# Kernel optimization log

Hardware: AMD Instinct MI355X
Metric: run time of the kernel (lower is better)

Reference implementation:

```python
import jax, jax.numpy as jnp
import numpy as np

ALPHA = 0.25
GAMMA = 2.0
W_CLASS = W_BBOX = W_GIOU = W_MASK = W_DICE = W_PROJ = 1.0
EPS = 1e-8


def box_cxcywh_to_xyxy(b):
    cx, cy, w, h = jnp.split(b, 4, axis=-1)
    return jnp.concatenate([cx - 0.5 * w, cy - 0.5 * h, cx + 0.5 * w, cy + 0.5 * h], axis=-1)


def dice_coef(inputs, targets):
    # inputs: logits [N, D]; targets: binary [M, D]
    s = jax.nn.sigmoid(inputs)
    num = 2.0 * jnp.einsum('nd,md->nm', s, targets)
    den = s.sum(-1)[:, None] + targets.sum(-1)[None, :]
    return (num + 1.0) / (den + 1.0)  # [N, M]


def sigmoid_focal_coef(inputs, targets):
    # inputs: logits [N, D]; targets: binary [M, D] -> [N, M]
    x = inputs[:, None, :]
    t = targets[None, :, :]
    p = jax.nn.sigmoid(x)
    # BCE-with-logits, numerically stable
    ce = jnp.maximum(x, 0.0) - x * t + jnp.log1p(jnp.exp(-jnp.abs(x)))
    p_t = p * t + (1.0 - p) * (1.0 - t)
    alpha_t = ALPHA * t + (1.0 - ALPHA) * (1.0 - t)
    return (alpha_t * ce * (1.0 - p_t) ** GAMMA).mean(-1)


def giou_cost(src_xyxy, tgt_xyxy):
    # src [nf, nq, 4], tgt [nf, 1, 4] -> cost [nf, nq, 1]
    a1 = (src_xyxy[..., 2] - src_xyxy[..., 0]) * (src_xyxy[..., 3] - src_xyxy[..., 1])
    a2 = (tgt_xyxy[..., 2] - tgt_xyxy[..., 0]) * (tgt_xyxy[..., 3] - tgt_xyxy[..., 1])
    lt = jnp.maximum(src_xyxy[:, :, None, :2], tgt_xyxy[:, None, :, :2])
    rb = jnp.minimum(src_xyxy[:, :, None, 2:], tgt_xyxy[:, None, :, 2:])
    wh = jnp.clip(rb - lt, 0.0)
    inter = wh[..., 0] * wh[..., 1]
    union = a1[:, :, None] + a2[:, None, :] - inter
    iou = inter / union
    ltc = jnp.minimum(src_xyxy[:, :, None, :2], tgt_xyxy[:, None, :, :2])
    rbc = jnp.maximum(src_xyxy[:, :, None, 2:], tgt_xyxy[:, None, :, 2:])
    whc = jnp.clip(rbc - ltc, 0.0)
    areac = whc[..., 0] * whc[..., 1]
    giou = iou - (areac - union) / areac
    return -giou


def cost_matrix_one(logits, boxes, masks, tmask, tbox, tvalid):
    # logits [nf,nq,1], boxes [nf,nq,4], masks [nf,nq,H,W], tmask [nf,H,W], tbox [nf,4], tvalid [nf]
    p = jax.nn.sigmoid(logits[..., 0])  # [nf, nq]
    neg = (1.0 - ALPHA) * p ** GAMMA * (-jnp.log(1.0 - p + EPS))
    pos = ALPHA * (1.0 - p) ** GAMMA * (-jnp.log(p + EPS))
    w = (tvalid != 0).astype(p.dtype)  # valid-frame mask replaces python `continue`
    cost_class = (((pos - neg) * w[:, None]).sum(0) / w.sum())[:, None]  # [nq, 1]

    cost_bbox = jnp.abs(boxes[:, :, None, :] - tbox[:, None, None, :]).sum(-1).mean(0)  # [nq, 1]
    cost_giou = giou_cost(box_cxcywh_to_xyxy(boxes), box_cxcywh_to_xyxy(tbox[:, None, :])).mean(0)

    out_mask = jnp.transpose(masks, (1, 0, 2, 3))  # [nq, nf, H, W]
    nq = out_mask.shape[0]
    flat_src = out_mask.reshape(nq, -1)
    flat_tgt = tmask.reshape(1, -1)
    cost_mask = sigmoid_focal_coef(flat_src, flat_tgt)  # [nq, 1]
    cost_dice = -dice_coef(flat_src, flat_tgt)

    src_y = jnp.max(out_mask, axis=2, keepdims=True).reshape(nq, -1)  # [nq, nf*W]
    src_x = jnp.max(out_mask, axis=3, keepdims=True).reshape(nq, -1)  # [nq, nf*H]
    tgt_y = jnp.max(tmask[None], axis=2, keepdims=True).reshape(1, -1)
    tgt_x = jnp.max(tmask[None], axis=3, keepdims=True).reshape(1, -1)
    cost_proj = -0.5 * (dice_coef(src_y, tgt_y) + dice_coef(src_x, tgt_x))

    C = (W_CLASS * cost_class + W_BBOX * cost_bbox + W_GIOU * cost_giou
         + W_MASK * cost_mask + W_DICE * cost_dice + W_PROJ * cost_proj)
    return C  # [nq, 1]


def setup_inputs() -> dict:
    key = jax.random.key(0)
    k = jax.random.split(key, 6)
    bs, nf, nq, H, W = 2, 8, 300, 96, 96
    pred_logits = jax.random.normal(k[0], (bs, nf, nq, 1), dtype=jnp.float32)
    pred_boxes = jax.random.uniform(k[1], (bs, nf, nq, 4), dtype=jnp.float32)
    pred_masks = jax.random.normal(k[2], (bs, nf, nq, H, W), dtype=jnp.float32)
    target_masks = (jax.random.uniform(k[3], (bs, nf, H, W)) < 0.3).astype(jnp.float32)
    tgt_boxes = jax.random.uniform(k[4], (bs, nf, 4), dtype=jnp.float32)
    tgt_valid = jnp.ones((bs, nf), dtype=jnp.int32)
    valid_pad = jnp.zeros((bs, H, W), dtype=bool)
    return {"pred_logits": pred_logits, "pred_boxes": pred_boxes, "pred_masks": pred_masks,
            "target_masks": target_masks, "tgt_boxes": tgt_boxes, "tgt_valid": tgt_valid,
            "valid_pad": valid_pad}


def reference(pred_logits, pred_boxes, pred_masks, target_masks, tgt_boxes, tgt_valid, valid_pad):
    # zero out predictions over padded regions (masked_fill with valid[:, None, None])
    masks = jnp.where(valid_pad[:, None, None, :, :], 0.0, pred_masks)
    C = jax.vmap(cost_matrix_one)(pred_logits, pred_boxes, masks, target_masks, tgt_boxes, tgt_valid)
    src_ind = jnp.argmin(C, axis=1).astype(jnp.int64)  # [bs, 1]
    tgt_ind = jnp.zeros_like(src_ind)
    return C, src_ind, tgt_ind
```

## Files before the change

### kernel.cpp

```cpp
#include <hip/hip_runtime.h>
#include <math.h>

#define NF 8
#define NQ 300
#define HSZ 96
#define WSZ 96
#define HW (HSZ*WSZ)
#define DTOT (NF*HW)
#define NT 256
#define NBF 16

#define WS_TGTY 0
#define WS_TGTX 1536
#define WS_TSUM 3072
#define WS_YSUM 3088
#define WS_XSUM 3104
#define WS_PART 4096

__device__ __forceinline__ float sigmoid_fast(float x) {
    float e = __expf(-fabsf(x));
    float inv = __builtin_amdgcn_rcpf(1.f + e);
    return x >= 0.f ? inv : e * inv;
}

__device__ __forceinline__ float blockSum(float v, float* red) {
    #pragma unroll
    for (int off = 32; off > 0; off >>= 1) v += __shfl_down(v, off, 64);
    int wid = threadIdx.x >> 6, lane = threadIdx.x & 63;
    __syncthreads();
    if (lane == 0) red[wid] = v;
    __syncthreads();
    return red[0] + red[1] + red[2] + red[3];
}

__global__ __launch_bounds__(NT)
void targets_kernel(const float* __restrict__ tm, float* __restrict__ ws) {
    int bf = blockIdx.x, t = threadIdx.x;
    __shared__ float tile[HSZ * 97];
    __shared__ float red[4];
    const float* base = tm + (size_t)bf * HW;
    float tsum = 0.f;
    #pragma unroll
    for (int it = 0; it < 36; ++it) {
        int e = it * NT + t;
        float v = base[e];
        tsum += v;
        tile[e + e / 96] = v;
    }
    __syncthreads();
    float ysum = 0.f, xsum = 0.f;
    if (t < 96) {
        float m = -INFINITY;
        #pragma unroll 8
        for (int h = 0; h < HSZ; ++h) m = fmaxf(m, tile[h * 97 + t]);
        ws[WS_TGTY + bf * 96 + t] = m;
        ysum = m;
    } else if (t < 192) {
        int hh = t - 96;
        float m = -INFINITY;
        #pragma unroll 8
        for (int w = 0; w < WSZ; ++w) m = fmaxf(m, tile[hh * 97 + w]);
        ws[WS_TGTX + bf * 96 + hh] = m;
        xsum = m;
    }
    tsum = blockSum(tsum, red);
    ysum = blockSum(ysum, red);
    xsum = blockSum(xsum, red);
    if (t == 0) {
        ws[WS_TSUM + bf] = tsum;
        ws[WS_YSUM + bf] = ysum;
        ws[WS_XSUM + bf] = xsum;
    }
}

__global__ __launch_bounds__(NT, 8)
void partial_kernel(const float* __restrict__ masks, const float* __restrict__ tmask,
                    const unsigned char* __restrict__ vpad, const float* __restrict__ ws,
                    float* __restrict__ part) {
    int bf = blockIdx.x / NQ;
    int q  = blockIdx.x - bf * NQ;
    int b  = bf >> 3;
    int t  = threadIdx.x;

    __shared__ unsigned short tile[HSZ * 98];
    __shared__ float red[4];

    const float4* mrow = (const float4*)(masks + (size_t)(bf * NQ + q) * HW);
    const float4* trow = (const float4*)(tmask + (size_t)bf * HW);
    const unsigned* prow = (const unsigned*)(vpad + (size_t)b * HW);

    float focal = 0.f, dnum = 0.f, dden = 0.f;

    #pragma unroll
    for (int it = 0; it < 9; ++it) {
        int i4 = it * NT + t;
        float4 xv = mrow[i4];
        float4 tv = trow[i4];
        unsigned pv = prow[i4];
        int h = i4 / 24;
        int c = (i4 - h * 24) * 4;

        float xs[4] = {xv.x, xv.y, xv.z, xv.w};
        float ts[4] = {tv.x, tv.y, tv.z, tv.w};
        unsigned short us[4];
        #pragma unroll
        for (int j = 0; j < 4; ++j) {
            float x = ((pv >> (8 * j)) & 0xFFu) ? 0.f : xs[j];
            float tg = ts[j];
            float ee = __expf(-fabsf(x));
            float se = 1.f + ee;
            float inv = __builtin_amdgcn_rcpf(se);
            float s = x >= 0.f ? inv : ee * inv;
            float L = __logf(se);
            float ce = fmaxf(x, 0.f) - x * tg + L;
            float omp = s + tg - 2.f * s * tg;
            float at = 0.75f - 0.5f * tg;
            focal = fmaf(at * ce, omp * omp, focal);
            dnum = fmaf(s, tg, dnum);
            dden += s;
            us[j] = (unsigned short)(__float_as_uint(x) >> 16);
        }
        int ta = h * 98 + c;
        *(unsigned*)&tile[ta]     = (unsigned)us[0] | ((unsigned)us[1] << 16);
        *(unsigned*)&tile[ta + 2] = (unsigned)us[2] | ((unsigned)us[3] << 16);
    }
    __syncthreads();

    float pYn = 0.f, pYd = 0.f, pXn = 0.f, pXd = 0.f;
    if (t < 96) {
        float m = -INFINITY;
        #pragma unroll 8
        for (int h = 0; h < HSZ; ++h)
            m = fmaxf(m, __uint_as_float((unsigned)tile[h * 98 + t] << 16));
        float sg = sigmoid_fast(m);
        pYd = sg;
        pYn = sg * ws[WS_TGTY + bf * 96 + t];
    } else if (t < 192) {
        int hh = t - 96;
        float m = -INFINITY;
        #pragma unroll 8
        for (int w = 0; w < WSZ; ++w)
            m = fmaxf(m, __uint_as_float((unsigned)tile[hh * 98 + w] << 16));
        float sg = sigmoid_fast(m);
        pXd = sg;
        pXn = sg * ws[WS_TGTX + bf * 96 + hh];
    }

    focal = blockSum(focal, red);
    dnum  = blockSum(dnum, red);
    dden  = blockSum(dden, red);
    pYn   = blockSum(pYn, red);
    pYd   = blockSum(pYd, red);
    pXn   = blockSum(pXn, red);
    pXd   = blockSum(pXd, red);

    if (t == 0) {
        float* p = part + (size_t)blockIdx.x * 8;
        p[0] = focal; p[1] = dnum; p[2] = dden;
        p[3] = pYn;   p[4] = pYd;  p[5] = pXn;  p[6] = pXd;
    }
}

__global__ __launch_bounds__(NT)
void combine_kernel(const float* __restrict__ logits, const float* __restrict__ boxes,
                    const float* __restrict__ tbox, const int* __restrict__ tvalid,
                    const float* __restrict__ ws, float* __restrict__ out) {
    int gid = blockIdx.x * NT + threadIdx.x;
    if (gid >= 2 * NQ) return;
    int b = gid / NQ, q = gid - b * NQ;

    float focal = 0.f, dnum = 0.f, dden = 0.f;
    float pYn = 0.f, pYd = 0.f, pXn = 0.f, pXd = 0.f;
    float tsum = 0.f, ysum = 0.f, xsum = 0.f;
    #pragma unroll
    for (int f = 0; f < NF; ++f) {
        int bf = b * NF + f;
        const float* p = ws + WS_PART + (size_t)(bf * NQ + q) * 8;
        focal += p[0]; dnum += p[1]; dden += p[2];
        pYn += p[3]; pYd += p[4]; pXn += p[5]; pXd += p[6];
        tsum += ws[WS_TSUM + bf];
        ysum += ws[WS_YSUM + bf];
        xsum += ws[WS_XSUM + bf];
    }
    float cost_mask = focal / (float)DTOT;
    float cost_dice = -(2.f * dnum + 1.f) / (dden + tsum + 1.f);
    float coefY = (2.f * pYn + 1.f) / (pYd + ysum + 1.f);
    float coefX = (2.f * pXn + 1.f) / (pXd + xsum + 1.f);
    float cost_proj = -0.5f * (coefY + coefX);

    float wsum = 0.f, cls = 0.f, cb = 0.f, cg = 0.f;
    #pragma unroll
    for (int f = 0; f < NF; ++f) {
        float wv = (tvalid[b * NF + f] != 0) ? 1.f : 0.f;
        wsum += wv;
        float lg = logits[(b * NF + f) * NQ + q];
        float p = sigmoid_fast(lg);
        float negc = 0.75f * p * p * (-__logf(1.f - p + 1e-8f));
        float posc = 0.25f * (1.f - p) * (1.f - p) * (-__logf(p + 1e-8f));
        cls += (posc - negc) * wv;

        const float* bx = boxes + (size_t)((b * NF + f) * NQ + q) * 4;
        const float* tb = tbox + (b * NF + f) * 4;
        float cx = bx[0], cy = bx[1], bw = bx[2], bh = bx[3];
        float tcx = tb[0], tcy = tb[1], tbw = tb[2], tbh = tb[3];
        cb += fabsf(cx - tcx) + fabsf(cy - tcy) + fabsf(bw - tbw) + fabsf(bh - tbh);
        float sx1 = cx - 0.5f * bw, sy1 = cy - 0.5f * bh;
        float sx2 = cx + 0.5f * bw, sy2 = cy + 0.5f * bh;
        float tx1 = tcx - 0.5f * tbw, ty1 = tcy - 0.5f * tbh;
        float tx2 = tcx + 0.5f * tbw, ty2 = tcy + 0.5f * tbh;
        float a1 = (sx2 - sx1) * (sy2 - sy1), a2 = (tx2 - tx1) * (ty2 - ty1);
        float iw = fmaxf(fminf(sx2, tx2) - fmaxf(sx1, tx1), 0.f);
        float ih = fmaxf(fminf(sy2, ty2) - fmaxf(sy1, ty1), 0.f);
        float inter = iw * ih;
        float uni = a1 + a2 - inter;
        float iou = inter / uni;
        float cw = fmaxf(fmaxf(sx2, tx2) - fminf(sx1, tx1), 0.f);
        float chh = fmaxf(fmaxf(sy2, ty2) - fminf(sy1, ty1), 0.f);
        float areac = cw * chh;
        cg += -(iou - (areac - uni) / areac);
    }
    cls /= wsum;
    cb *= 0.125f;
    cg *= 0.125f;
    out[b * NQ + q] = cls + cb + cg + cost_mask + cost_dice + cost_proj;
}

__global__ __launch_bounds__(NT)
void argmin_kernel(float* __restrict__ out, int write_idx) {
    int b = blockIdx.x, t = threadIdx.x;
    float best = INFINITY;
    int bi = 0x7fffffff;
    for (int q = t; q < NQ; q += NT) {
        float v = out[b * NQ + q];
        if (v < best) { best = v; bi = q; }
    }
    #pragma unroll
    for (int off = 32; off > 0; off >>= 1) {
        float ov = __shfl_down(best, off, 64);
        int oi = __shfl_down(bi, off, 64);
        if (ov < best || (ov == best && oi < bi)) { best = ov; bi = oi; }
    }
    __shared__ float rv[4];
    __shared__ int ri[4];
    int wid = t >> 6, lane = t & 63;
    if (lane == 0) { rv[wid] = best; ri[wid] = bi; }
    __syncthreads();
    if (t == 0 && write_idx) {
        #pragma unroll
        for (int w = 1; w < 4; ++w) {
            if (rv[w] < best || (rv[w] == best && ri[w] < bi)) { best = rv[w]; bi = ri[w]; }
        }
        out[2 * NQ + b] = (float)bi;
        out[2 * NQ + 2 + b] = 0.f;
    }
}

extern "C" void kernel_launch(void* const* d_in, const int* in_sizes, int n_in,
                              void* d_out, int out_size, void* d_ws, size_t ws_size,
                              hipStream_t stream) {
    const float* logits = (const float*)d_in[0];
    const float* boxes  = (const float*)d_in[1];
    const float* masks  = (const float*)d_in[2];
    const float* tmask  = (const float*)d_in[3];
    const float* tbox   = (const float*)d_in[4];
    const int*   tvalid = (const int*)d_in[5];
    const unsigned char* vpad = (const unsigned char*)d_in[6];
    float* out = (float*)d_out;
    float* ws  = (float*)d_ws;

    targets_kernel<<<NBF, NT, 0, stream>>>(tmask, ws);
    partial_kernel<<<NBF * NQ, NT, 0, stream>>>(masks, tmask, vpad, ws, ws + WS_PART);
    combine_kernel<<<(2 * NQ + NT - 1) / NT, NT, 0, stream>>>(logits, boxes, tbox,
                                                              tvalid, ws, out);
    int write_idx = (out_size >= 2 * NQ + 4) ? 1 : 0;
    argmin_kernel<<<2, NT, 0, stream>>>(out, write_idx);
}
```

Baseline: 311.8 us.

## Bit-pack target and pad masks, batch reductions, merge combine with argmin

The targets kernel now also packs the binary target masks and padding masks into bitmasks using wave ballots. The partial kernel then reads these bits instead of full float targets and byte pad values, which is meant to cut its per-block global traffic to mostly the prediction masks. All nine float4 mask loads are issued up front, and the seven block reductions are batched into one shared-memory sync round. The combine and argmin kernels are fused into one two-block kernel, removing a launch but serialising the combine work over only 2 blocks.

```diff
diff --git a/kernel.cpp b/kernel.cpp
--- a/kernel.cpp
+++ b/kernel.cpp
@@ -5,8 +5,8 @@
 #define NQ 300
 #define HSZ 96
 #define WSZ 96
-#define HW (HSZ*WSZ)
-#define DTOT (NF*HW)
+#define HW 9216
+#define DTOT 73728
 #define NT 256
 #define NBF 16
 
@@ -15,7 +15,9 @@
 #define WS_TSUM 3072
 #define WS_YSUM 3088
 #define WS_XSUM 3104
-#define WS_PART 4096
+#define WS_TBITS 3200
+#define WS_PBITS 7808
+#define WS_PART  8448
 
 __device__ __forceinline__ float sigmoid_fast(float x) {
     float e = __expf(-fabsf(x));
@@ -23,21 +25,14 @@
     return x >= 0.f ? inv : e * inv;
 }
 
-__device__ __forceinline__ float blockSum(float v, float* red) {
-    #pragma unroll
-    for (int off = 32; off > 0; off >>= 1) v += __shfl_down(v, off, 64);
-    int wid = threadIdx.x >> 6, lane = threadIdx.x & 63;
-    __syncthreads();
-    if (lane == 0) red[wid] = v;
-    __syncthreads();
-    return red[0] + red[1] + red[2] + red[3];
-}
-
 __global__ __launch_bounds__(NT)
-void targets_kernel(const float* __restrict__ tm, float* __restrict__ ws) {
+void targets_kernel(const float* __restrict__ tm, const unsigned char* __restrict__ vpad,
+                    float* __restrict__ ws) {
     int bf = blockIdx.x, t = threadIdx.x;
+    int lane = t & 63, wv = t >> 6;
     __shared__ float tile[HSZ * 97];
-    __shared__ float red[4];
+    __shared__ float red[4][4];
+    unsigned long long* tb64 = (unsigned long long*)(ws + WS_TBITS) + bf * 144;
     const float* base = tm + (size_t)bf * HW;
     float tsum = 0.f;
     #pragma unroll
@@ -45,7 +40,20 @@
         int e = it * NT + t;
         float v = base[e];
         tsum += v;
+        unsigned long long bt = __ballot(v != 0.f);
+        if (lane == 0) tb64[it * 4 + wv] = bt;
         tile[e + e / 96] = v;
+    }
+    if ((bf & 7) == 0) {
+        int b = bf >> 3;
+        unsigned long long* pb64 = (unsigned long long*)(ws + WS_PBITS) + b * 144;
+        const unsigned char* pp = vpad + (size_t)b * HW;
+        #pragma unroll
+        for (int it = 0; it < 36; ++it) {
+            int e = it * NT + t;
+            unsigned long long bt = __ballot(pp[e] != 0);
+            if (lane == 0) pb64[it * 4 + wv] = bt;
+        }
     }
     __syncthreads();
     float ysum = 0.f, xsum = 0.f;
@@ -63,50 +71,63 @@
         ws[WS_TGTX + bf * 96 + hh] = m;
         xsum = m;
     }
-    tsum = blockSum(tsum, red);
-    ysum = blockSum(ysum, red);
-    xsum = blockSum(xsum, red);
+    float v0 = tsum, v1 = ysum, v2 = xsum;
+    #pragma unroll
+    for (int off = 32; off > 0; off >>= 1) {
+        v0 += __shfl_down(v0, off, 64);
+        v1 += __shfl_down(v1, off, 64);
+        v2 += __shfl_down(v2, off, 64);
+    }
+    if (lane == 0) { red[wv][0] = v0; red[wv][1] = v1; red[wv][2] = v2; }
+    __syncthreads();
     if (t == 0) {
-        ws[WS_TSUM + bf] = tsum;
-        ws[WS_YSUM + bf] = ysum;
-        ws[WS_XSUM + bf] = xsum;
+        #pragma unroll
+        for (int w = 1; w < 4; ++w) { v0 += red[w][0]; v1 += red[w][1]; v2 += red[w][2]; }
+        ws[WS_TSUM + bf] = v0;
+        ws[WS_YSUM + bf] = v1;
+        ws[WS_XSUM + bf] = v2;
     }
 }
 
 __global__ __launch_bounds__(NT, 8)
-void partial_kernel(const float* __restrict__ masks, const float* __restrict__ tmask,
-                    const unsigned char* __restrict__ vpad, const float* __restrict__ ws,
+void partial_kernel(const float* __restrict__ masks, const float* __restrict__ ws,
                     float* __restrict__ part) {
-    int bf = blockIdx.x / NQ;
-    int q  = blockIdx.x - bf * NQ;
+    int blk = blockIdx.x;
+    int bf = blk / NQ;
+    int q  = blk - bf * NQ;
     int b  = bf >> 3;
     int t  = threadIdx.x;
 
     __shared__ unsigned short tile[HSZ * 98];
-    __shared__ float red[4];
+    __shared__ float red[4][8];
 
     const float4* mrow = (const float4*)(masks + (size_t)(bf * NQ + q) * HW);
-    const float4* trow = (const float4*)(tmask + (size_t)bf * HW);
-    const unsigned* prow = (const unsigned*)(vpad + (size_t)b * HW);
+    const unsigned* tb = (const unsigned*)(ws + WS_TBITS) + bf * 288;
+    const unsigned* pb = (const unsigned*)(ws + WS_PBITS) + b * 288;
+
+    float4 xv[9];
+    #pragma unroll
+    for (int it = 0; it < 9; ++it) xv[it] = mrow[it * NT + t];
+
+    int widx = t >> 3;
+    int sh = (t & 7) * 4;
 
     float focal = 0.f, dnum = 0.f, dden = 0.f;
 
     #pragma unroll
     for (int it = 0; it < 9; ++it) {
         int i4 = it * NT + t;
-        float4 xv = mrow[i4];
-        float4 tv = trow[i4];
-        unsigned pv = prow[i4];
+        unsigned tw = tb[it * 32 + widx] >> sh;
+        unsigned pw = pb[it * 32 + widx] >> sh;
         int h = i4 / 24;
         int c = (i4 - h * 24) * 4;
 
-        float xs[4] = {xv.x, xv.y, xv.z, xv.w};
-        float ts[4] = {tv.x, tv.y, tv.z, tv.w};
-        unsigned short us[4];
+        float xs[4] = {xv[it].x, xv[it].y, xv[it].z, xv[it].w};
+        unsigned us[4];
         #pragma unroll
         for (int j = 0; j < 4; ++j) {
-            float x = ((pv >> (8 * j)) & 0xFFu) ? 0.f : xs[j];
-            float tg = ts[j];
+            float x = ((pw >> j) & 1u) ? 0.f : xs[j];
+            float tg = (float)((tw >> j) & 1u);
             float ee = __expf(-fabsf(x));
             float se = 1.f + ee;
             float inv = __builtin_amdgcn_rcpf(se);
@@ -118,11 +139,11 @@
             focal = fmaf(at * ce, omp * omp, focal);
             dnum = fmaf(s, tg, dnum);
             dden += s;
-            us[j] = (unsigned short)(__float_as_uint(x) >> 16);
+            us[j] = __float_as_uint(x) >> 16;
         }
         int ta = h * 98 + c;
-        *(unsigned*)&tile[ta]     = (unsigned)us[0] | ((unsigned)us[1] << 16);
-        *(unsigned*)&tile[ta + 2] = (unsigned)us[2] | ((unsigned)us[3] << 16);
+        *(unsigned*)&tile[ta]     = us[0] | (us[1] << 16);
+        *(unsigned*)&tile[ta + 2] = us[2] | (us[3] << 16);
     }
     __syncthreads();
 
@@ -146,94 +167,96 @@
         pXn = sg * ws[WS_TGTX + bf * 96 + hh];
     }
 
-    focal = blockSum(focal, red);
-    dnum  = blockSum(dnum, red);
-    dden  = blockSum(dden, red);
-    pYn   = blockSum(pYn, red);
-    pYd   = blockSum(pYd, red);
-    pXn   = blockSum(pXn, red);
-    pXd   = blockSum(pXd, red);
-
+    float v[7] = {focal, dnum, dden, pYn, pYd, pXn, pXd};
+    #pragma unroll
+    for (int k = 0; k < 7; ++k)
+        #pragma unroll
+        for (int off = 32; off > 0; off >>= 1) v[k] += __shfl_down(v[k], off, 64);
+    int wv = t >> 6, lane = t & 63;
+    if (lane == 0) {
+        #pragma unroll
+        for (int k = 0; k < 7; ++k) red[wv][k] = v[k];
+    }
+    __syncthreads();
     if (t == 0) {
-        float* p = part + (size_t)blockIdx.x * 8;
-        p[0] = focal; p[1] = dnum; p[2] = dden;
-        p[3] = pYn;   p[4] = pYd;  p[5] = pXn;  p[6] = pXd;
+        #pragma unroll
+        for (int w = 1; w < 4; ++w)
+            #pragma unroll
+            for (int k = 0; k < 7; ++k) v[k] += red[w][k];
+        float4* p = (float4*)(part + (size_t)blk * 8);
+        p[0] = make_float4(v[0], v[1], v[2], v[3]);
+        p[1] = make_float4(v[4], v[5], v[6], 0.f);
     }
 }
 
 __global__ __launch_bounds__(NT)
-void combine_kernel(const float* __restrict__ logits, const float* __restrict__ boxes,
-                    const float* __restrict__ tbox, const int* __restrict__ tvalid,
-                    const float* __restrict__ ws, float* __restrict__ out) {
-    int gid = blockIdx.x * NT + threadIdx.x;
-    if (gid >= 2 * NQ) return;
-    int b = gid / NQ, q = gid - b * NQ;
-
-    float focal = 0.f, dnum = 0.f, dden = 0.f;
-    float pYn = 0.f, pYd = 0.f, pXn = 0.f, pXd = 0.f;
-    float tsum = 0.f, ysum = 0.f, xsum = 0.f;
-    #pragma unroll
-    for (int f = 0; f < NF; ++f) {
-        int bf = b * NF + f;
-        const float* p = ws + WS_PART + (size_t)(bf * NQ + q) * 8;
-        focal += p[0]; dnum += p[1]; dden += p[2];
-        pYn += p[3]; pYd += p[4]; pXn += p[5]; pXd += p[6];
-        tsum += ws[WS_TSUM + bf];
-        ysum += ws[WS_YSUM + bf];
-        xsum += ws[WS_XSUM + bf];
-    }
-    float cost_mask = focal / (float)DTOT;
-    float cost_dice = -(2.f * dnum + 1.f) / (dden + tsum + 1.f);
-    float coefY = (2.f * pYn + 1.f) / (pYd + ysum + 1.f);
-    float coefX = (2.f * pXn + 1.f) / (pXd + xsum + 1.f);
-    float cost_proj = -0.5f * (coefY + coefX);
-
-    float wsum = 0.f, cls = 0.f, cb = 0.f, cg = 0.f;
-    #pragma unroll
-    for (int f = 0; f < NF; ++f) {
-        float wv = (tvalid[b * NF + f] != 0) ? 1.f : 0.f;
-        wsum += wv;
-        float lg = logits[(b * NF + f) * NQ + q];
-        float p = sigmoid_fast(lg);
-        float negc = 0.75f * p * p * (-__logf(1.f - p + 1e-8f));
-        float posc = 0.25f * (1.f - p) * (1.f - p) * (-__logf(p + 1e-8f));
-        cls += (posc - negc) * wv;
-
-        const float* bx = boxes + (size_t)((b * NF + f) * NQ + q) * 4;
-        const float* tb = tbox + (b * NF + f) * 4;
-        float cx = bx[0], cy = bx[1], bw = bx[2], bh = bx[3];
-        float tcx = tb[0], tcy = tb[1], tbw = tb[2], tbh = tb[3];
-        cb += fabsf(cx - tcx) + fabsf(cy - tcy) + fabsf(bw - tbw) + fabsf(bh - tbh);
-        float sx1 = cx - 0.5f * bw, sy1 = cy - 0.5f * bh;
-        float sx2 = cx + 0.5f * bw, sy2 = cy + 0.5f * bh;
-        float tx1 = tcx - 0.5f * tbw, ty1 = tcy - 0.5f * tbh;
-        float tx2 = tcx + 0.5f * tbw, ty2 = tcy + 0.5f * tbh;
-        float a1 = (sx2 - sx1) * (sy2 - sy1), a2 = (tx2 - tx1) * (ty2 - ty1);
-        float iw = fmaxf(fminf(sx2, tx2) - fmaxf(sx1, tx1), 0.f);
-        float ih = fmaxf(fminf(sy2, ty2) - fmaxf(sy1, ty1), 0.f);
-        float inter = iw * ih;
-        float uni = a1 + a2 - inter;
-        float iou = inter / uni;
-        float cw = fmaxf(fmaxf(sx2, tx2) - fminf(sx1, tx1), 0.f);
-        float chh = fmaxf(fmaxf(sy2, ty2) - fminf(sy1, ty1), 0.f);
-        float areac = cw * chh;
-        cg += -(iou - (areac - uni) / areac);
-    }
-    cls /= wsum;
-    cb *= 0.125f;
-    cg *= 0.125f;
-    out[b * NQ + q] = cls + cb + cg + cost_mask + cost_dice + cost_proj;
-}
-
-__global__ __launch_bounds__(NT)
-void argmin_kernel(float* __restrict__ out, int write_idx) {
+void final_kernel(const float* __restrict__ logits, const float* __restrict__ boxes,
+                  const float* __restrict__ tbox, const int* __restrict__ tvalid,
+                  const float* __restrict__ ws, float* __restrict__ out, int write_idx) {
     int b = blockIdx.x, t = threadIdx.x;
+    const float* part = ws + WS_PART;
+
     float best = INFINITY;
     int bi = 0x7fffffff;
+
     for (int q = t; q < NQ; q += NT) {
-        float v = out[b * NQ + q];
-        if (v < best) { best = v; bi = q; }
-    }
+        float focal = 0.f, dnum = 0.f, dden = 0.f;
+        float pYn = 0.f, pYd = 0.f, pXn = 0.f, pXd = 0.f;
+        float tsum = 0.f, ysum = 0.f, xsum = 0.f;
+        #pragma unroll
+        for (int f = 0; f < NF; ++f) {
+            int bf = b * NF + f;
+            const float4* p = (const float4*)(part + (size_t)(bf * NQ + q) * 8);
+            float4 pa = p[0], pbv = p[1];
+            focal += pa.x; dnum += pa.y; dden += pa.z; pYn += pa.w;
+            pYd += pbv.x; pXn += pbv.y; pXd += pbv.z;
+            tsum += ws[WS_TSUM + bf];
+            ysum += ws[WS_YSUM + bf];
+            xsum += ws[WS_XSUM + bf];
+        }
+        float cost_mask = focal / (float)DTOT;
+        float cost_dice = -(2.f * dnum + 1.f) / (dden + tsum + 1.f);
+        float coefY = (2.f * pYn + 1.f) / (pYd + ysum + 1.f);
+        float coefX = (2.f * pXn + 1.f) / (pXd + xsum + 1.f);
+        float cost_proj = -0.5f * (coefY + coefX);
+
+        float wsum = 0.f, cls = 0.f, cb = 0.f, cg = 0.f;
+        #pragma unroll
+        for (int f = 0; f < NF; ++f) {
+            float wv = (tvalid[b * NF + f] != 0) ? 1.f : 0.f;
+            wsum += wv;
+            float lg = logits[(b * NF + f) * NQ + q];
+            float p = sigmoid_fast(lg);
+            float negc = 0.75f * p * p * (-__logf(1.f - p + 1e-8f));
+            float posc = 0.25f * (1.f - p) * (1.f - p) * (-__logf(p + 1e-8f));
+            cls += (posc - negc) * wv;
+
+            const float* bx = boxes + (size_t)((b * NF + f) * NQ + q) * 4;
+            const float* tbp = tbox + (b * NF + f) * 4;
+            float cx = bx[0], cy = bx[1], bw = bx[2], bh = bx[3];
+            float tcx = tbp[0], tcy = tbp[1], tbw = tbp[2], tbh = tbp[3];
+            cb += fabsf(cx - tcx) + fabsf(cy - tcy) + fabsf(bw - tbw) + fabsf(bh - tbh);
+            float sx1 = cx - 0.5f * bw, sy1 = cy - 0.5f * bh;
+            float sx2 = cx + 0.5f * bw, sy2 = cy + 0.5f * bh;
+            float tx1 = tcx - 0.5f * tbw, ty1 = tcy - 0.5f * tbh;
+            float tx2 = tcx + 0.5f * tbw, ty2 = tcy + 0.5f * tbh;
+            float a1 = (sx2 - sx1) * (sy2 - sy1), a2 = (tx2 - tx1) * (ty2 - ty1);
+            float iw = fmaxf(fminf(sx2, tx2) - fmaxf(sx1, tx1), 0.f);
+            float ih = fmaxf(fminf(sy2, ty2) - fmaxf(sy1, ty1), 0.f);
+            float inter = iw * ih;
+            float uni = a1 + a2 - inter;
+            float iou = inter / uni;
+            float cw = fmaxf(fmaxf(sx2, tx2) - fminf(sx1, tx1), 0.f);
+            float chh = fmaxf(fmaxf(sy2, ty2) - fminf(sy1, ty1), 0.f);
+            float areac = cw * chh;
+            cg += -(iou - (areac - uni) / areac);
+        }
+        cls /= wsum;
+        float c = cls + 0.125f * cb + 0.125f * cg + cost_mask + cost_dice + cost_proj;
+        out[b * NQ + q] = c;
+        if (c < best) { best = c; bi = q; }
+    }
+
     #pragma unroll
     for (int off = 32; off > 0; off >>= 1) {
         float ov = __shfl_down(best, off, 64);
@@ -242,8 +265,8 @@
     }
     __shared__ float rv[4];
     __shared__ int ri[4];
-    int wid = t >> 6, lane = t & 63;
-    if (lane == 0) { rv[wid] = best; ri[wid] = bi; }
+    int wv = t >> 6, lane = t & 63;
+    if (lane == 0) { rv[wv] = best; ri[wv] = bi; }
     __syncthreads();
     if (t == 0 && write_idx) {
         #pragma unroll
@@ -268,10 +291,8 @@
     float* out = (float*)d_out;
     float* ws  = (float*)d_ws;
 
-    targets_kernel<<<NBF, NT, 0, stream>>>(tmask, ws);
-    partial_kernel<<<NBF * NQ, NT, 0, stream>>>(masks, tmask, vpad, ws, ws + WS_PART);
-    combine_kernel<<<(2 * NQ + NT - 1) / NT, NT, 0, stream>>>(logits, boxes, tbox,
-                                                              tvalid, ws, out);
+    targets_kernel<<<NBF, NT, 0, stream>>>(tmask, vpad, ws);
+    partial_kernel<<<NBF * NQ, NT, 0, stream>>>(masks, ws, ws + WS_PART);
     int write_idx = (out_size >= 2 * NQ + 4) ? 1 : 0;
-    argmin_kernel<<<2, NT, 0, stream>>>(out, write_idx);
-}
+    final_kernel<<<2, NT, 0, stream>>>(logits, boxes, tbox, tvalid, ws, out, write_idx);
+}
```

After: 464.5 us. 49.0% more time.
